# Performance work log

Measured on AMD Instinct MI355X. Metric: run time of the kernel, lower is better.

The kernel has to match this reference:

```python
import jax, jax.numpy as jnp
import numpy as np

N = 100000      # nodes
E = 1600000     # edges
IN = 4          # input_size
H = 128         # hidden_channels
R = 20          # num_robots
OUT = 2         # output_size


def setup_inputs() -> dict:
    key = jax.random.key(0)
    ks = jax.random.split(key, 9)
    x = jax.random.normal(ks[0], (N, IN), dtype=jnp.float32)
    edge_index = jax.random.randint(ks[1], (2, E), 0, N, dtype=jnp.int32)
    batch = jnp.zeros((N,), dtype=jnp.int32)  # single graph
    # GCNConv weights (glorot-ish) and biases
    W1 = jax.random.normal(ks[2], (IN, H), dtype=jnp.float32) / np.sqrt(IN)
    b1 = jnp.zeros((H,), dtype=jnp.float32)
    W2 = jax.random.normal(ks[3], (H, H), dtype=jnp.float32) / np.sqrt(H)
    b2 = jnp.zeros((H,), dtype=jnp.float32)
    Wfc = jax.random.normal(ks[4], (H, OUT * R), dtype=jnp.float32) / np.sqrt(H)
    bfc = jnp.zeros((OUT * R,), dtype=jnp.float32)
    return {"x": x, "edge_index": edge_index, "batch": batch,
            "W1": W1, "b1": b1, "W2": W2, "b2": b2, "Wfc": Wfc, "bfc": bfc}


def gcn_conv(x, W, b, src, dst, n):
    # PyG GCNConv: h = x @ W, symmetric deg^-1/2 norm (self-loops already in src/dst),
    # aggregate messages at dst, then add bias.
    h = x @ W                                                     # [n, H_out]
    deg = jax.ops.segment_sum(jnp.ones(src.shape[0], h.dtype), dst, num_segments=n)
    dinv = jnp.where(deg > 0, jax.lax.rsqrt(deg), 0.0)            # [n]
    norm = dinv[src] * dinv[dst]                                  # [E+n]
    out = jax.ops.segment_sum(h[src] * norm[:, None], dst, num_segments=n)
    return out + b


def reference(x, edge_index, batch, W1, b1, W2, b2, Wfc, bfc):
    n = x.shape[0]
    loops = jnp.arange(n, dtype=edge_index.dtype)
    src = jnp.concatenate([edge_index[0], loops])   # add self-loops (GCNConv default)
    dst = jnp.concatenate([edge_index[1], loops])

    h = jnp.tanh(gcn_conv(x, W1, b1, src, dst, n))
    h = jnp.tanh(gcn_conv(h, W2, b2, src, dst, n))

    # global_mean_pool over batch (single graph)
    num_graphs = 1
    sums = jax.ops.segment_sum(h, batch, num_segments=num_graphs)           # [G, H]
    cnt = jax.ops.segment_sum(jnp.ones((n,), h.dtype), batch, num_segments=num_graphs)
    pooled = sums / jnp.maximum(cnt, 1.0)[:, None]

    vel = (pooled @ Wfc + bfc).reshape(-1, R, OUT)                          # [G, R, 2]

    # in_size = number of nodes with both first two features nonzero
    in_size = jnp.sum((x[:, 0] != 0.0) & (x[:, 1] != 0.0))
    mask = (jnp.arange(R) < in_size)[None, :, None]
    return jnp.where(mask, vel, 0.0)
```

## Files before the change

### kernel.cpp

```cpp
#include <hip/hip_runtime.h>
#include <hip/hip_fp16.h>

#define NN 100000
#define NE 1600000
#define INF 4
#define H 128
#define RR 20
#define OUTF 2
#define NB 782
#define NBP 784
#define EPB 16384
#define NBLK ((NE + EPB - 1) / EPB)

typedef unsigned int uint32;
typedef __attribute__((ext_vector_type(8))) short short8;
typedef __attribute__((ext_vector_type(4))) float f32x4;

__device__ inline uint32 pack_f16(float x, float y) {
    return (uint32)__half_as_ushort(__float2half(x)) |
           ((uint32)__half_as_ushort(__float2half(y)) << 16);
}
__device__ inline __half2 bc_h2(uint32 u) {
    union { uint32 u; __half2 h; } c; c.u = u; return c.h;
}

__global__ void k_init_small(float* __restrict__ pooled, int* __restrict__ in_size) {
    int t = threadIdx.x;
    if (t < H) pooled[t] = 0.f;
    if (t == H) *in_size = 0;
}

__global__ void k_init_nodes(const float* __restrict__ x, int* __restrict__ in_size) {
    int i = blockIdx.x * 256 + threadIdx.x;
    bool pred = false;
    if (i < NN) {
        float x0 = x[(size_t)i * INF + 0];
        float x1 = x[(size_t)i * INF + 1];
        pred = (x0 != 0.f) && (x1 != 0.f);
    }
    unsigned long long m = __ballot(pred);
    if ((threadIdx.x & 63) == 0) {
        int c = __popcll(m);
        if (c) atomicAdd(in_size, c);
    }
}

__global__ void __launch_bounds__(256) k_hist(const int* __restrict__ dst,
                                              int* __restrict__ histG) {
    __shared__ int h[NB];
    int b = blockIdx.x, t = threadIdx.x;
    for (int i = t; i < NB; i += 256) h[i] = 0;
    __syncthreads();
    int e0 = b * EPB, eend = min(e0 + EPB, NE);
    for (int e = e0 + t; e < eend; e += 256) atomicAdd(&h[dst[e] >> 7], 1);
    __syncthreads();
    for (int i = t; i < NB; i += 256) histG[b * NBP + i] = h[i];
}

__global__ void k_btotoffs(const int* __restrict__ histG, int* __restrict__ offs,
                           int* __restrict__ btot) {
    int bkt = blockIdx.x * 256 + threadIdx.x;
    if (bkt >= NB) return;
    int run = 0;
    for (int j = 0; j < NBLK; ++j) {
        int v = histG[j * NBP + bkt];
        offs[j * NBP + bkt] = run;
        run += v;
    }
    btot[bkt] = run;
}

__global__ void __launch_bounds__(1024) k_bbase(const int* __restrict__ btot,
                                                int* __restrict__ bbase) {
    __shared__ int sm[1024];
    int t = threadIdx.x;
    int v = (t < NB) ? btot[t] : 0;
    sm[t] = v;
    __syncthreads();
    for (int off = 1; off < 1024; off <<= 1) {
        int u = (t >= off) ? sm[t - off] : 0;
        __syncthreads();
        sm[t] += u;
        __syncthreads();
    }
    if (t < NB) bbase[t] = sm[t] - v;
    if (t == 0) bbase[NB] = NE;
}

__global__ void __launch_bounds__(256) k_scat2(const int* __restrict__ src,
                                               const int* __restrict__ dst,
                                               const int* __restrict__ offs,
                                               const int* __restrict__ bbase,
                                               uint32* __restrict__ data) {
    __shared__ int cur[NB];
    int b = blockIdx.x, t = threadIdx.x;
    for (int i = t; i < NB; i += 256) cur[i] = offs[b * NBP + i] + bbase[i];
    __syncthreads();
    int e0 = b * EPB, eend = min(e0 + EPB, NE);
    for (int e = e0 + t; e < eend; e += 256) {
        int s = src[e], d = dst[e];
        int p = atomicAdd(&cur[d >> 7], 1);
        data[p] = ((uint32)s << 7) | (uint32)(d & 127);
    }
}

__global__ void __launch_bounds__(256) k_build(const uint32* __restrict__ data,
                                               const int* __restrict__ bbase,
                                               int* __restrict__ csr_off,
                                               int* __restrict__ csr_cnt,
                                               int* __restrict__ csr_src,
                                               float* __restrict__ dinv) {
    __shared__ int hist[128], pfx[128], curs[128];
    int bkt = blockIdx.x;
    int t = threadIdx.x;
    int rbeg = bbase[bkt], rend = bbase[bkt + 1];
    if (t < 128) hist[t] = 0;
    __syncthreads();
    for (int j = rbeg + t; j < rend; j += 256)
        atomicAdd(&hist[data[j] & 127], 1);
    __syncthreads();
    if (t < 128) pfx[t] = hist[t];
    __syncthreads();
    for (int off = 1; off < 128; off <<= 1) {
        int u = (t < 128 && t >= off) ? pfx[t - off] : 0;
        __syncthreads();
        if (t < 128) pfx[t] += u;
        __syncthreads();
    }
    int nodeCount = min(128, NN - bkt * 128);
    if (t < nodeCount) {
        int excl = rbeg + pfx[t] - hist[t];
        csr_off[bkt * 128 + t] = excl;
        csr_cnt[bkt * 128 + t] = hist[t];
        curs[t] = excl;
        dinv[bkt * 128 + t] = rsqrtf((float)(hist[t] + 1));
    }
    __syncthreads();
    for (int j = rbeg + t; j < rend; j += 256) {
        uint32 r = data[j];
        int p = atomicAdd(&curs[r & 127], 1);
        csr_src[p] = (int)(r >> 7);
    }
}

__global__ void __launch_bounds__(256) k_aggmm1(const uint32* __restrict__ data,
                                                const int* __restrict__ bbase,
                                                const float* __restrict__ x,
                                                const float* __restrict__ dinv,
                                                const float* __restrict__ W1,
                                                const float* __restrict__ b1,
                                                uint32* __restrict__ Yp) {
    __shared__ float acc[128][4];
    __shared__ float w1s[4][128];
    __shared__ float b1s[128];
    int bkt = blockIdx.x;
    int t = threadIdx.x;
    if (t < 128) {
        acc[t][0] = 0.f; acc[t][1] = 0.f; acc[t][2] = 0.f; acc[t][3] = 0.f;
        b1s[t] = b1[t];
    }
    ((float*)w1s)[t] = W1[t];
    ((float*)w1s)[256 + t] = W1[256 + t];
    int rbeg = bbase[bkt], rend = bbase[bkt + 1];
    __syncthreads();
    for (int j = rbeg + t; j < rend; j += 256) {
        uint32 r = data[j];
        int s = (int)(r >> 7), dl = (int)(r & 127);
        float w = dinv[s];
        const float4 xv = *(const float4*)(x + (size_t)s * INF);
        atomicAdd(&acc[dl][0], xv.x * w);
        atomicAdd(&acc[dl][1], xv.y * w);
        atomicAdd(&acc[dl][2], xv.z * w);
        atomicAdd(&acc[dl][3], xv.w * w);
    }
    __syncthreads();
    int nbase = bkt * 128;
    #pragma unroll
    for (int rep = 0; rep < 32; ++rep) {
        int flat = rep * 256 + t;
        int node = flat >> 6;
        int fp = flat & 63;
        int gi = nbase + node;
        if (gi < NN) {
            float di = dinv[gi];
            const float4 xi = *(const float4*)(x + (size_t)gi * INF);
            float a0 = (acc[node][0] + xi.x * di) * di;
            float a1 = (acc[node][1] + xi.y * di) * di;
            float a2 = (acc[node][2] + xi.z * di) * di;
            float a3 = (acc[node][3] + xi.w * di) * di;
            int f0 = fp * 2;
            float d0 = b1s[f0]     + a0 * w1s[0][f0]     + a1 * w1s[1][f0]
                                   + a2 * w1s[2][f0]     + a3 * w1s[3][f0];
            float d1 = b1s[f0 + 1] + a0 * w1s[0][f0 + 1] + a1 * w1s[1][f0 + 1]
                                   + a2 * w1s[2][f0 + 1] + a3 * w1s[3][f0 + 1];
            Yp[(size_t)gi * 64 + fp] = pack_f16(tanhf(d0) * di, tanhf(d1) * di);
        }
    }
}

__global__ void k_aggy(const uint32* __restrict__ Yp, const int* __restrict__ csr_off,
                       const int* __restrict__ csr_cnt, const int* __restrict__ csr_src,
                       const float* __restrict__ dinv, uint32* __restrict__ Zp) {
    int wid = threadIdx.x >> 6;
    int lane = threadIdx.x & 63;
    int i = blockIdx.x * 4 + wid;
    if (i >= NN) return;
    int b = csr_off[i];
    int n = csr_cnt[i];
    int eg = lane >> 4, seg = lane & 15;

    __half2 h0 = bc_h2(0u), h1 = bc_h2(0u), h2 = bc_h2(0u), h3 = bc_h2(0u);
    int j = 0;
    for (; j + 8 <= n; j += 8) {
        int s0 = csr_src[b + j + eg];
        int s1 = csr_src[b + j + 4 + eg];
        uint4 v0 = *(const uint4*)(Yp + (size_t)s0 * 64 + seg * 4);
        uint4 v1 = *(const uint4*)(Yp + (size_t)s1 * 64 + seg * 4);
        h0 = __hadd2(h0, bc_h2(v0.x)); h1 = __hadd2(h1, bc_h2(v0.y));
        h2 = __hadd2(h2, bc_h2(v0.z)); h3 = __hadd2(h3, bc_h2(v0.w));
        h0 = __hadd2(h0, bc_h2(v1.x)); h1 = __hadd2(h1, bc_h2(v1.y));
        h2 = __hadd2(h2, bc_h2(v1.z)); h3 = __hadd2(h3, bc_h2(v1.w));
    }
    for (; j < n; j += 4) {
        int jj = j + eg;
        bool valid = jj < n;
        int s = valid ? csr_src[b + jj] : i;
        uint4 v = *(const uint4*)(Yp + (size_t)s * 64 + seg * 4);
        if (valid) {
            h0 = __hadd2(h0, bc_h2(v.x)); h1 = __hadd2(h1, bc_h2(v.y));
            h2 = __hadd2(h2, bc_h2(v.z)); h3 = __hadd2(h3, bc_h2(v.w));
        }
    }
    {
        uint4 v = *(const uint4*)(Yp + (size_t)i * 64 + seg * 4);
        if (eg == 0) {
            h0 = __hadd2(h0, bc_h2(v.x)); h1 = __hadd2(h1, bc_h2(v.y));
            h2 = __hadd2(h2, bc_h2(v.z)); h3 = __hadd2(h3, bc_h2(v.w));
        }
    }
    float a[8];
    { float2 f = __half22float2(h0); a[0] = f.x; a[1] = f.y; }
    { float2 f = __half22float2(h1); a[2] = f.x; a[3] = f.y; }
    { float2 f = __half22float2(h2); a[4] = f.x; a[5] = f.y; }
    { float2 f = __half22float2(h3); a[6] = f.x; a[7] = f.y; }
    #pragma unroll
    for (int m = 0; m < 8; ++m) {
        a[m] += __shfl_xor(a[m], 16, 64);
        a[m] += __shfl_xor(a[m], 32, 64);
    }
    if (eg == 0) {
        float di = dinv[i];
        uint4 o;
        o.x = pack_f16(a[0] * di, a[1] * di);
        o.y = pack_f16(a[2] * di, a[3] * di);
        o.z = pack_f16(a[4] * di, a[5] * di);
        o.w = pack_f16(a[6] * di, a[7] * di);
        *(uint4*)(Zp + (size_t)i * 64 + seg * 4) = o;
    }
}

__global__ void __launch_bounds__(256) k_mm2pool(
    const uint32* __restrict__ Zp, const float* __restrict__ W2,
    const float* __restrict__ b2, float* __restrict__ pooled) {
    int tid = threadIdx.x;
    int wid = tid >> 6, lane = tid & 63;
    int nsub = lane & 15;
    int kg = lane >> 4;
    int fbase = wid * 32;

    short8 Bh[2][4], Bl[2][4];
    #pragma unroll
    for (int c = 0; c < 2; ++c) {
        #pragma unroll
        for (int ks = 0; ks < 4; ++ks) {
            short8 h, l;
            #pragma unroll
            for (int i = 0; i < 8; ++i) {
                float w = W2[(size_t)(ks * 32 + kg * 8 + i) * H + (fbase + c * 16 + nsub)];
                __half hh = __float2half(w);
                float wl = w - __half2float(hh);
                __half hl = __float2half(wl);
                h[i] = (short)__half_as_ushort(hh);
                l[i] = (short)__half_as_ushort(hl);
            }
            Bh[c][ks] = h;
            Bl[c][ks] = l;
        }
    }
    float bb0 = b2[fbase + nsub];
    float bb1 = b2[fbase + 16 + nsub];
    float pool0 = 0.f, pool1 = 0.f;

    const int ntiles = NN / 16;
    const int stride = (int)gridDim.x;
    int t = (int)blockIdx.x;

    short8 A[4];
    if (t < ntiles) {
        const uint32* rp = Zp + (size_t)(t * 16 + nsub) * 64 + kg * 4;
        #pragma unroll
        for (int ks = 0; ks < 4; ++ks) A[ks] = *(const short8*)(rp + ks * 16);
    }
    while (t < ntiles) {
        int tn = t + stride;
        short8 An[4];
        if (tn < ntiles) {
            const uint32* rp = Zp + (size_t)(tn * 16 + nsub) * 64 + kg * 4;
            #pragma unroll
            for (int ks = 0; ks < 4; ++ks) An[ks] = *(const short8*)(rp + ks * 16);
        }
        {
            f32x4 acch0 = {0.f,0.f,0.f,0.f}, accl0 = {0.f,0.f,0.f,0.f};
            f32x4 acch1 = {0.f,0.f,0.f,0.f}, accl1 = {0.f,0.f,0.f,0.f};
            #pragma unroll
            for (int ks = 0; ks < 4; ++ks) {
                acch0 = __builtin_amdgcn_mfma_f32_16x16x32_f16(A[ks], Bh[0][ks], acch0, 0, 0, 0);
                accl0 = __builtin_amdgcn_mfma_f32_16x16x32_f16(A[ks], Bl[0][ks], accl0, 0, 0, 0);
                acch1 = __builtin_amdgcn_mfma_f32_16x16x32_f16(A[ks], Bh[1][ks], acch1, 0, 0, 0);
                accl1 = __builtin_amdgcn_mfma_f32_16x16x32_f16(A[ks], Bl[1][ks], accl1, 0, 0, 0);
            }
            #pragma unroll
            for (int r = 0; r < 4; ++r) {
                pool0 += tanhf(acch0[r] + accl0[r] + bb0);
                pool1 += tanhf(acch1[r] + accl1[r] + bb1);
            }
        }
        #pragma unroll
        for (int ks = 0; ks < 4; ++ks) A[ks] = An[ks];
        t = tn;
    }

    pool0 += __shfl_xor(pool0, 16, 64);
    pool0 += __shfl_xor(pool0, 32, 64);
    pool1 += __shfl_xor(pool1, 16, 64);
    pool1 += __shfl_xor(pool1, 32, 64);
    if (kg == 0) {
        atomicAdd(&pooled[fbase + nsub], pool0);
        atomicAdd(&pooled[fbase + 16 + nsub], pool1);
    }
}

__global__ void k_final(const float* __restrict__ pooled, const float* __restrict__ Wfc,
                        const float* __restrict__ bfc, const int* __restrict__ in_size,
                        float* __restrict__ out) {
    int t = threadIdx.x;
    if (t >= RR * OUTF) return;
    const float invn = 1.0f / (float)NN;
    float a = bfc[t];
    for (int k = 0; k < H; ++k) a += (pooled[k] * invn) * Wfc[k * (RR * OUTF) + t];
    int r = t >> 1;
    out[t] = (r < *in_size) ? a : 0.f;
}

extern "C" void kernel_launch(void* const* d_in, const int* in_sizes, int n_in,
                              void* d_out, int out_size, void* d_ws, size_t ws_size,
                              hipStream_t stream) {
    const float* x   = (const float*)d_in[0];
    const int*   ei  = (const int*)d_in[1];
    const float* W1  = (const float*)d_in[3];
    const float* b1  = (const float*)d_in[4];
    const float* W2  = (const float*)d_in[5];
    const float* b2  = (const float*)d_in[6];
    const float* Wfc = (const float*)d_in[7];
    const float* bfc = (const float*)d_in[8];
    float* out = (float*)d_out;

    const int* srcp = ei;
    const int* dstp = ei + NE;

    char* ws = (char*)d_ws;
    size_t off = 0;
    auto alloc = [&](size_t bytes) { void* p = ws + off; off += (bytes + 511) & ~(size_t)511; return p; };
    int*    histG   = (int*)alloc((size_t)NBLK * NBP * 4);
    int*    offs    = (int*)alloc((size_t)NBLK * NBP * 4);
    int*    btot    = (int*)alloc((size_t)NB * 4);
    int*    bbase   = (int*)alloc(((size_t)NB + 1) * 4);
    uint32* data    = (uint32*)alloc((size_t)NE * 4);
    float*  dinv    = (float*)alloc((size_t)NN * 4);
    int*    csr_off = (int*)alloc((size_t)NN * 4);
    int*    csr_cnt = (int*)alloc((size_t)NN * 4);
    int*    csr_src = (int*)alloc((size_t)NE * 4);
    uint32* Yp      = (uint32*)alloc((size_t)NN * 64 * 4);
    uint32* Zp      = (uint32*)alloc((size_t)NN * 64 * 4);
    float*  pooled  = (float*)alloc(H * 4);
    int*    in_size = (int*)alloc(64);
    (void)off; (void)ws_size; (void)in_sizes; (void)n_in; (void)out_size;

    const int nbN = (NN + 255) / 256;
    const int nbW = (NN + 3) / 4;

    k_init_small<<<1, 256, 0, stream>>>(pooled, in_size);
    k_init_nodes<<<nbN, 256, 0, stream>>>(x, in_size);
    k_hist<<<NBLK, 256, 0, stream>>>(dstp, histG);
    k_btotoffs<<<(NB + 255) / 256, 256, 0, stream>>>(histG, offs, btot);
    k_bbase<<<1, 1024, 0, stream>>>(btot, bbase);
    k_scat2<<<NBLK, 256, 0, stream>>>(srcp, dstp, offs, bbase, data);
    k_build<<<NB, 256, 0, stream>>>(data, bbase, csr_off, csr_cnt, csr_src, dinv);
    k_aggmm1<<<NB, 256, 0, stream>>>(data, bbase, x, dinv, W1, b1, Yp);
    k_aggy<<<nbW, 256, 0, stream>>>(Yp, csr_off, csr_cnt, csr_src, dinv, Zp);
    k_mm2pool<<<512, 256, 0, stream>>>(Zp, W2, b2, pooled);
    k_final<<<1, 64, 0, stream>>>(pooled, Wfc, bfc, in_size, out);
}
```

Baseline: 319.3 us.

## Split layer-1 aggregation across four blocks per bucket and separate the mm1 stage

Precomputes x*dinv per node in the CSR build kernel so the layer-1 gather reads one float4 instead of x plus dinv. The per-bucket edge aggregation is split across four blocks, each writing partial sums that a new merge kernel combines with the self-loop term. The dense W1 transform and tanh then run in their own kernel with one wave per node. This raises parallelism (782 blocks become 3128) at the cost of two extra launches and extra global traffic for the partial and intermediate buffers.

```diff
diff --git a/kernel.cpp b/kernel.cpp
--- a/kernel.cpp
+++ b/kernel.cpp
@@ -11,6 +11,7 @@
 #define NBP 784
 #define EPB 16384
 #define NBLK ((NE + EPB - 1) / EPB)
+#define ASPLIT 4
 
 typedef unsigned int uint32;
 typedef __attribute__((ext_vector_type(8))) short short8;
@@ -106,10 +107,12 @@
 
 __global__ void __launch_bounds__(256) k_build(const uint32* __restrict__ data,
                                                const int* __restrict__ bbase,
+                                               const float* __restrict__ x,
                                                int* __restrict__ csr_off,
                                                int* __restrict__ csr_cnt,
                                                int* __restrict__ csr_src,
-                                               float* __restrict__ dinv) {
+                                               float* __restrict__ dinv,
+                                               float4* __restrict__ xd) {
     __shared__ int hist[128], pfx[128], curs[128];
     int bkt = blockIdx.x;
     int t = threadIdx.x;
@@ -129,11 +132,15 @@
     }
     int nodeCount = min(128, NN - bkt * 128);
     if (t < nodeCount) {
+        int gi = bkt * 128 + t;
         int excl = rbeg + pfx[t] - hist[t];
-        csr_off[bkt * 128 + t] = excl;
-        csr_cnt[bkt * 128 + t] = hist[t];
+        csr_off[gi] = excl;
+        csr_cnt[gi] = hist[t];
         curs[t] = excl;
-        dinv[bkt * 128 + t] = rsqrtf((float)(hist[t] + 1));
+        float di = rsqrtf((float)(hist[t] + 1));
+        dinv[gi] = di;
+        const float4 xv = *(const float4*)(x + (size_t)gi * INF);
+        xd[gi] = make_float4(xv.x * di, xv.y * di, xv.z * di, xv.w * di);
     }
     __syncthreads();
     for (int j = rbeg + t; j < rend; j += 256) {
@@ -143,59 +150,71 @@
     }
 }
 
-__global__ void __launch_bounds__(256) k_aggmm1(const uint32* __restrict__ data,
-                                                const int* __restrict__ bbase,
-                                                const float* __restrict__ x,
-                                                const float* __restrict__ dinv,
-                                                const float* __restrict__ W1,
-                                                const float* __restrict__ b1,
-                                                uint32* __restrict__ Yp) {
+__global__ void __launch_bounds__(256) k_aggx4(const uint32* __restrict__ data,
+                                               const int* __restrict__ bbase,
+                                               const float4* __restrict__ xd,
+                                               float* __restrict__ Axpart) {
     __shared__ float acc[128][4];
+    int bkt = blockIdx.x >> 2, sp = blockIdx.x & 3;
+    int t = threadIdx.x;
+    if (t < 128) { acc[t][0] = 0.f; acc[t][1] = 0.f; acc[t][2] = 0.f; acc[t][3] = 0.f; }
+    int rbeg = bbase[bkt], rend = bbase[bkt + 1];
+    int len = rend - rbeg;
+    int q0 = rbeg + ((long long)len * sp >> 2);
+    int q1 = rbeg + ((long long)len * (sp + 1) >> 2);
+    __syncthreads();
+    for (int j = q0 + t; j < q1; j += 256) {
+        uint32 r = data[j];
+        int s = (int)(r >> 7), dl = (int)(r & 127);
+        const float4 v = xd[s];
+        atomicAdd(&acc[dl][0], v.x);
+        atomicAdd(&acc[dl][1], v.y);
+        atomicAdd(&acc[dl][2], v.z);
+        atomicAdd(&acc[dl][3], v.w);
+    }
+    __syncthreads();
+    float* dstp = Axpart + (size_t)blockIdx.x * 512;
+    for (int i = t; i < 512; i += 256) dstp[i] = ((const float*)acc)[i];
+}
+
+__global__ void k_merge(const float* __restrict__ Axpart, const float4* __restrict__ xd,
+                        const float* __restrict__ dinv, float4* __restrict__ Ax) {
+    int i = blockIdx.x * 256 + threadIdx.x;
+    if (i >= NN) return;
+    int bkt = i >> 7, nl = i & 127;
+    float4 a = xd[i];
+    #pragma unroll
+    for (int sp = 0; sp < 4; ++sp) {
+        const float4 p = *(const float4*)(Axpart + ((size_t)(bkt * 4 + sp)) * 512 + nl * 4);
+        a.x += p.x; a.y += p.y; a.z += p.z; a.w += p.w;
+    }
+    float di = dinv[i];
+    Ax[i] = make_float4(a.x * di, a.y * di, a.z * di, a.w * di);
+}
+
+__global__ void __launch_bounds__(256) k_mm1b(const float4* __restrict__ Ax,
+                                              const float* __restrict__ dinv,
+                                              const float* __restrict__ W1,
+                                              const float* __restrict__ b1,
+                                              uint32* __restrict__ Yp) {
     __shared__ float w1s[4][128];
     __shared__ float b1s[128];
-    int bkt = blockIdx.x;
-    int t = threadIdx.x;
-    if (t < 128) {
-        acc[t][0] = 0.f; acc[t][1] = 0.f; acc[t][2] = 0.f; acc[t][3] = 0.f;
-        b1s[t] = b1[t];
-    }
+    int t = threadIdx.x;
+    if (t < 128) b1s[t] = b1[t];
     ((float*)w1s)[t] = W1[t];
     ((float*)w1s)[256 + t] = W1[256 + t];
-    int rbeg = bbase[bkt], rend = bbase[bkt + 1];
-    __syncthreads();
-    for (int j = rbeg + t; j < rend; j += 256) {
-        uint32 r = data[j];
-        int s = (int)(r >> 7), dl = (int)(r & 127);
-        float w = dinv[s];
-        const float4 xv = *(const float4*)(x + (size_t)s * INF);
-        atomicAdd(&acc[dl][0], xv.x * w);
-        atomicAdd(&acc[dl][1], xv.y * w);
-        atomicAdd(&acc[dl][2], xv.z * w);
-        atomicAdd(&acc[dl][3], xv.w * w);
-    }
-    __syncthreads();
-    int nbase = bkt * 128;
-    #pragma unroll
-    for (int rep = 0; rep < 32; ++rep) {
-        int flat = rep * 256 + t;
-        int node = flat >> 6;
-        int fp = flat & 63;
-        int gi = nbase + node;
-        if (gi < NN) {
-            float di = dinv[gi];
-            const float4 xi = *(const float4*)(x + (size_t)gi * INF);
-            float a0 = (acc[node][0] + xi.x * di) * di;
-            float a1 = (acc[node][1] + xi.y * di) * di;
-            float a2 = (acc[node][2] + xi.z * di) * di;
-            float a3 = (acc[node][3] + xi.w * di) * di;
-            int f0 = fp * 2;
-            float d0 = b1s[f0]     + a0 * w1s[0][f0]     + a1 * w1s[1][f0]
-                                   + a2 * w1s[2][f0]     + a3 * w1s[3][f0];
-            float d1 = b1s[f0 + 1] + a0 * w1s[0][f0 + 1] + a1 * w1s[1][f0 + 1]
-                                   + a2 * w1s[2][f0 + 1] + a3 * w1s[3][f0 + 1];
-            Yp[(size_t)gi * 64 + fp] = pack_f16(tanhf(d0) * di, tanhf(d1) * di);
-        }
-    }
+    __syncthreads();
+    int wid = t >> 6, lane = t & 63;
+    int node = blockIdx.x * 4 + wid;
+    if (node >= NN) return;
+    const float4 a = Ax[node];
+    float di = dinv[node];
+    int f0 = lane * 2;
+    float d0 = b1s[f0]     + a.x * w1s[0][f0]     + a.y * w1s[1][f0]
+                           + a.z * w1s[2][f0]     + a.w * w1s[3][f0];
+    float d1 = b1s[f0 + 1] + a.x * w1s[0][f0 + 1] + a.y * w1s[1][f0 + 1]
+                           + a.z * w1s[2][f0 + 1] + a.w * w1s[3][f0 + 1];
+    Yp[(size_t)node * 64 + lane] = pack_f16(tanhf(d0) * di, tanhf(d1) * di);
 }
 
 __global__ void k_aggy(const uint32* __restrict__ Yp, const int* __restrict__ csr_off,
@@ -377,9 +396,12 @@
     int*    bbase   = (int*)alloc(((size_t)NB + 1) * 4);
     uint32* data    = (uint32*)alloc((size_t)NE * 4);
     float*  dinv    = (float*)alloc((size_t)NN * 4);
+    float4* xd      = (float4*)alloc((size_t)NN * 16);
     int*    csr_off = (int*)alloc((size_t)NN * 4);
     int*    csr_cnt = (int*)alloc((size_t)NN * 4);
     int*    csr_src = (int*)alloc((size_t)NE * 4);
+    float*  Axpart  = (float*)alloc((size_t)NB * ASPLIT * 512 * 4);
+    float4* Ax      = (float4*)alloc((size_t)NN * 16);
     uint32* Yp      = (uint32*)alloc((size_t)NN * 64 * 4);
     uint32* Zp      = (uint32*)alloc((size_t)NN * 64 * 4);
     float*  pooled  = (float*)alloc(H * 4);
@@ -395,8 +417,10 @@
     k_btotoffs<<<(NB + 255) / 256, 256, 0, stream>>>(histG, offs, btot);
     k_bbase<<<1, 1024, 0, stream>>>(btot, bbase);
     k_scat2<<<NBLK, 256, 0, stream>>>(srcp, dstp, offs, bbase, data);
-    k_build<<<NB, 256, 0, stream>>>(data, bbase, csr_off, csr_cnt, csr_src, dinv);
-    k_aggmm1<<<NB, 256, 0, stream>>>(data, bbase, x, dinv, W1, b1, Yp);
+    k_build<<<NB, 256, 0, stream>>>(data, bbase, x, csr_off, csr_cnt, csr_src, dinv, xd);
+    k_aggx4<<<NB * ASPLIT, 256, 0, stream>>>(data, bbase, xd, Axpart);
+    k_merge<<<nbN, 256, 0, stream>>>(Axpart, xd, dinv, Ax);
+    k_mm1b<<<nbW, 256, 0, stream>>>(Ax, dinv, W1, b1, Yp);
     k_aggy<<<nbW, 256, 0, stream>>>(Yp, csr_off, csr_cnt, csr_src, dinv, Zp);
     k_mm2pool<<<512, 256, 0, stream>>>(Zp, W2, b2, pooled);
     k_final<<<1, 64, 0, stream>>>(pooled, Wfc, bfc, in_size, out);
```

New measurement: 316.0 us. About the same (-1.0%).
